# Performance work log

Measured on AMD Instinct MI355X. Metric: run time of the kernel, lower is better.

Reference implementation:

```python
import jax, jax.numpy as jnp
import numpy as np

N_NODES = 50000
N_EDGES = 1600000
D = 64  # per-node feature dim for h1 and h2


def setup_inputs() -> dict:
    key = jax.random.key(0)
    ks = jax.random.split(key, 8)
    h1 = jax.random.normal(ks[0], (N_NODES, D), dtype=jnp.float32)
    h2 = jax.random.normal(ks[1], (N_NODES, D), dtype=jnp.float32)
    src = jax.random.randint(ks[2], (N_EDGES,), 0, N_NODES)
    dst = jax.random.randint(ks[3], (N_EDGES,), 0, N_NODES)
    # MLP params: layer_sizes = [256, 128, 128, 1]
    def glorot(k, fan_in, fan_out):
        lim = (6.0 / (fan_in + fan_out)) ** 0.5
        return jax.random.uniform(k, (fan_in, fan_out), jnp.float32, -lim, lim)
    W0 = glorot(ks[4], 4 * D, 128)
    W1 = glorot(ks[5], 128, 128)
    W2 = glorot(ks[6], 128, 1)
    b0 = jnp.zeros((128,), jnp.float32)
    b1 = jnp.zeros((128,), jnp.float32)
    b2 = jnp.zeros((1,), jnp.float32)
    return {"h1": h1, "h2": h2, "src": src, "dst": dst,
            "W0": W0, "b0": b0, "W1": W1, "b1": b1, "W2": W2, "b2": b2}


def reference(h1, h2, src, dst, W0, b0, W1, b1, W2, b2):
    # Edge-wise gather of src/dst node features, concat -> MLP (eval mode: dropout=identity).
    h = jnp.concatenate([h1[src], h1[dst], h2[src], h2[dst]], axis=1)  # [E, 4D]
    h = h @ W0 + b0
    h = jax.nn.relu(h) @ W1 + b1
    h = jax.nn.relu(h) @ W2 + b2
    return h  # [E, out_features]
```

## Files before the change

kernel.cpp:

```cpp
#include <hip/hip_runtime.h>
#include <hip/hip_bf16.h>
#include <stdint.h>


typedef __attribute__((ext_vector_type(8))) __bf16 bf16x8;
typedef __attribute__((ext_vector_type(4))) __bf16 bf16x4;
typedef __attribute__((ext_vector_type(4))) float  floatx4;

__device__ inline floatx4 mfma16x16x32(bf16x8 a, bf16x8 b, floatx4 c) {
  return __builtin_amdgcn_mfma_f32_16x16x32_bf16(a, b, c, 0, 0, 0);
}

__device__ inline void bar_lds() {
  asm volatile("s_waitcnt lgkmcnt(0)" ::: "memory");
  __builtin_amdgcn_s_barrier();
}

__global__ void cvt_w_kernel(const float* __restrict__ W0, const float* __restrict__ W1,
                             __bf16* __restrict__ W1T, __bf16* __restrict__ W0uT,
                             __bf16* __restrict__ W0wT) {
  const int t = blockIdx.x * 256 + threadIdx.x;
  if (t < 16384) {
    const int n = t >> 7, k = t & 127;
    W1T[t] = (__bf16)W1[k * 128 + n];
  } else if (t < 32768) {
    const int t2 = t - 16384;
    const int n = t2 >> 7, k2 = t2 & 127;
    const int row = (k2 < 64) ? k2 : 64 + k2;
    W0uT[t2] = (__bf16)W0[row * 128 + n];
  } else {
    const int t3 = t - 32768;
    const int n = t3 >> 7, k2 = t3 & 127;
    const int row = (k2 < 64) ? 64 + k2 : 128 + k2;
    W0wT[t3] = (__bf16)W0[row * 128 + n];
  }
}

__global__ __launch_bounds__(256, 2)
void node_uw_kernel(const float* __restrict__ h1, const float* __restrict__ h2,
                    const __bf16* __restrict__ W0uT, const __bf16* __restrict__ W0wT,
                    const float* __restrict__ b0,
                    __bf16* __restrict__ uTab, __bf16* __restrict__ wTab, int nNodes) {
  __shared__ char sN[64 * 256];
  const int tid = threadIdx.x;
  const int base = blockIdx.x * 64;

  {
    const int r = tid >> 2, q = tid & 3;
    const int node = base + r;
    const int swz = (r & 7) << 4;
#pragma unroll
    for (int ii = 0; ii < 4; ++ii) {
      const int c = q * 4 + ii;
      bf16x8 v;
      if (node < nNodes) {
        const float* sp = (c < 8) ? (h1 + (size_t)node * 64 + c * 8)
                                  : (h2 + (size_t)node * 64 + (c - 8) * 8);
        const float4 x = reinterpret_cast<const float4*>(sp)[0];
        const float4 y = reinterpret_cast<const float4*>(sp)[1];
        v[0] = (__bf16)x.x; v[1] = (__bf16)x.y; v[2] = (__bf16)x.z; v[3] = (__bf16)x.w;
        v[4] = (__bf16)y.x; v[5] = (__bf16)y.y; v[6] = (__bf16)y.z; v[7] = (__bf16)y.w;
      } else {
#pragma unroll
        for (int k = 0; k < 8; ++k) v[k] = (__bf16)0.f;
      }
      *reinterpret_cast<bf16x8*>(sN + r * 256 + ((c * 16) ^ swz)) = v;
    }
  }
  __syncthreads();

  const int lane = tid & 63;
  const int l15 = lane & 15;
  const int hi = lane >> 4;
  const int hi16 = hi * 16;
  const int wvU = __builtin_amdgcn_readfirstlane(tid >> 6);

  float b0c[2][4];
#pragma unroll
  for (int nt = 0; nt < 2; ++nt)
#pragma unroll
    for (int r = 0; r < 4; ++r) b0c[nt][r] = b0[wvU * 32 + nt * 16 + hi * 4 + r];

#pragma unroll
  for (int pass = 0; pass < 2; ++pass) {
    const __bf16* Wt = pass ? W0wT : W0uT;
    __bf16* Tab = pass ? wTab : uTab;
    const bf16x8* wp = reinterpret_cast<const bf16x8*>(Wt);
    bf16x8 wf[4][2];
#pragma unroll
    for (int kk = 0; kk < 4; ++kk) {
      wf[kk][0] = wp[(wvU * 32 + l15) * 16 + kk * 4 + hi];
      wf[kk][1] = wp[(wvU * 32 + 16 + l15) * 16 + kk * 4 + hi];
    }
    floatx4 acc[4][2];
#pragma unroll
    for (int mt = 0; mt < 4; ++mt) { acc[mt][0] = (floatx4)0.f; acc[mt][1] = (floatx4)0.f; }
#pragma unroll
    for (int kk = 0; kk < 4; ++kk) {
#pragma unroll
      for (int mt = 0; mt < 4; ++mt) {
        const int row = mt * 16 + l15;
        const bf16x8 a = *reinterpret_cast<const bf16x8*>(
            sN + row * 256 + ((kk * 64 + hi16) ^ ((row & 7) << 4)));
        acc[mt][0] = mfma16x16x32(wf[kk][0], a, acc[mt][0]);
        acc[mt][1] = mfma16x16x32(wf[kk][1], a, acc[mt][1]);
      }
    }
#pragma unroll
    for (int mt = 0; mt < 4; ++mt) {
      const int node = base + mt * 16 + l15;
      if (node < nNodes) {
#pragma unroll
        for (int nt = 0; nt < 2; ++nt) {
          bf16x4 pk;
#pragma unroll
          for (int r = 0; r < 4; ++r) {
            const float v = acc[mt][nt][r] + (pass ? 0.f : b0c[nt][r]);
            pk[r] = (__bf16)v;
          }
          *reinterpret_cast<bf16x4*>(Tab + (size_t)node * 128 + wvU * 32 + nt * 16 +
                                     hi * 4) = pk;
        }
      }
    }
  }
}

__global__ __launch_bounds__(512, 2)
void edge_uw_kernel(const __bf16* __restrict__ uTab, const __bf16* __restrict__ wTab,
                    const int* __restrict__ srcI, const int* __restrict__ dstI,
                    const __bf16* __restrict__ W1T, const float* __restrict__ b1,
                    const float* __restrict__ W2, const float* __restrict__ b2,
                    float* __restrict__ out, int E, int nTiles) {
  __shared__ char sUW[2 * 64 * 512];
  __shared__ char sH[64 * 256];

  const int tid = threadIdx.x;
  const int lane = tid & 63;
  const int l15 = lane & 15;
  const int hi = lane >> 4;
  const int hi16 = hi * 16;
  const int wvU = __builtin_amdgcn_readfirstlane(tid >> 6);
  const int wm = wvU >> 2;
  const int wn = wvU & 3;
  const int wvByte = wvU * 4096;

  const int lhalf = lane >> 5;
  const int p31 = lane & 31;
  const int half = (p31 >> 4) & 1;
  const int* gIdxTab = half ? dstI : srcI;
  const __bf16* gTab = half ? wTab : uTab;

  bf16x8 w1f[4][2];
  const bf16x8* w1p = reinterpret_cast<const bf16x8*>(W1T);
#pragma unroll
  for (int kk = 0; kk < 4; ++kk) {
    w1f[kk][0] = w1p[(wn * 32 + l15) * 16 + kk * 4 + hi];
    w1f[kk][1] = w1p[(wn * 32 + 16 + l15) * 16 + kk * 4 + hi];
  }
  float b1c[2][4], w2c[2][4];
#pragma unroll
  for (int nt = 0; nt < 2; ++nt)
#pragma unroll
    for (int r = 0; r < 4; ++r) {
      const int n = wn * 32 + nt * 16 + hi * 4 + r;
      b1c[nt][r] = b1[n];
      w2c[nt][r] = W2[n];
    }
  const float b2v = b2[0];

  const int tstride = gridDim.x;

  auto loadIdx = [&](int (&d)[4], int tt2) {
    const bool valid = tt2 < nTiles;
#pragma unroll
    for (int i = 0; i < 4; ++i) {
      const int eLoc = wvU * 8 + i * 2 + lhalf;
      const int ge = tt2 * 64 + eLoc;
      d[i] = (valid && ge < E) ? gIdxTab[ge] : 0;
    }
  };

  auto issueGather = [&](int nb, const int (&idx4)[4]) {
#pragma unroll
    for (int i = 0; i < 4; ++i) {
      const int eLoc = wvU * 8 + i * 2 + lhalf;
      const int wc = (p31 & 8) | ((p31 & 7) ^ (eLoc & 7));
      const __bf16* g = gTab + (size_t)idx4[i] * 128 + wc * 8;
      char* l = sUW + nb * 32768 + wvByte + i * 1024;
      __builtin_amdgcn_global_load_lds(
          (const __attribute__((address_space(1))) void*)g,
          (__attribute__((address_space(3))) void*)l, 16, 0, 0);
    }
  };

  const int tile0 = blockIdx.x;
  int idxA[4], idxB[4];
  loadIdx(idxA, tile0);
  issueGather(0, idxA);
  loadIdx(idxB, tile0 + tstride);
  int cur = 0;

  for (int tt = tile0; tt < nTiles; tt += tstride) {
    __syncthreads();

    if (tt + tstride < nTiles) issueGather(cur ^ 1, idxB);
    loadIdx(idxA, tt + 2 * tstride);

    const char* sUWc = sUW + cur * 32768;

    {
      const int aR = tid >> 3;
      const int q = tid & 7;
      const int aswz = (aR & 7) << 4;
      const char* rowU = sUWc + aR * 512;
      char* rowH = sH + aR * 256;
#pragma unroll
      for (int ii = 0; ii < 2; ++ii) {
        const int c = q * 2 + ii;
        const int off = (c * 16) ^ aswz;
        const bf16x8 uu = *reinterpret_cast<const bf16x8*>(rowU + off);
        const bf16x8 ww = *reinterpret_cast<const bf16x8*>(rowU + 256 + off);
        bf16x8 hh;
#pragma unroll
        for (int k = 0; k < 8; ++k)
          hh[k] = (__bf16)fmaxf((float)uu[k] + (float)ww[k], 0.0f);
        *reinterpret_cast<bf16x8*>(rowH + off) = hh;
      }
    }
    bar_lds();

    floatx4 acc2T[2][2];
#pragma unroll
    for (int mt = 0; mt < 2; ++mt) { acc2T[mt][0] = (floatx4)0.f; acc2T[mt][1] = (floatx4)0.f; }
#pragma unroll
    for (int kk = 0; kk < 4; ++kk) {
#pragma unroll
      for (int mt = 0; mt < 2; ++mt) {
        const int row = wm * 32 + mt * 16 + l15;
        const bf16x8 a = *reinterpret_cast<const bf16x8*>(
            sH + row * 256 + ((kk * 64 + hi16) ^ ((row & 7) << 4)));
        acc2T[mt][0] = mfma16x16x32(w1f[kk][0], a, acc2T[mt][0]);
        acc2T[mt][1] = mfma16x16x32(w1f[kk][1], a, acc2T[mt][1]);
      }
    }

    float* sRedF = (float*)sUWc;
#pragma unroll
    for (int mt = 0; mt < 2; ++mt) {
      float pp = 0.f;
#pragma unroll
      for (int nt = 0; nt < 2; ++nt)
#pragma unroll
        for (int r = 0; r < 4; ++r)
          pp += fmaxf(acc2T[mt][nt][r] + b1c[nt][r], 0.0f) * w2c[nt][r];
      pp += __shfl_xor(pp, 16);
      pp += __shfl_xor(pp, 32);
      if (lane < 16) sRedF[(wm * 32 + mt * 16 + l15) * 4 + wn] = pp;
    }
    bar_lds();

    if (tid < 64) {
      const int ge = tt * 64 + tid;
      if (ge < E) {
        const float4 v = reinterpret_cast<const float4*>(sRedF)[tid];
        out[ge] = v.x + v.y + v.z + v.w + b2v;
      }
    }

#pragma unroll
    for (int i = 0; i < 4; ++i) idxB[i] = idxA[i];
    cur ^= 1;
  }
}

__global__ void edge_mlp_fallback(const float* __restrict__ h1, const float* __restrict__ h2,
                                  const int* __restrict__ src, const int* __restrict__ dst,
                                  const float* __restrict__ W0, const float* __restrict__ b0,
                                  const float* __restrict__ W1, const float* __restrict__ b1,
                                  const float* __restrict__ W2, const float* __restrict__ b2,
                                  float* __restrict__ out, int E) {
  __shared__ float sa[256];
  __shared__ float sh[128];
  __shared__ float sr[128];
  const int e = blockIdx.x;
  if (e >= E) return;
  const int t = threadIdx.x;
  const int is = src[e], id = dst[e];
  if (t < 64) { sa[t] = h1[is * 64 + t]; sa[128 + t] = h2[is * 64 + t]; }
  else { const int u = t - 64; sa[64 + u] = h1[id * 64 + u]; sa[192 + u] = h2[id * 64 + u]; }
  __syncthreads();
  float a0 = b0[t];
  for (int k = 0; k < 256; ++k) a0 += sa[k] * W0[k * 128 + t];
  sh[t] = fmaxf(a0, 0.f);
  __syncthreads();
  float a1 = b1[t];
  for (int k = 0; k < 128; ++k) a1 += sh[k] * W1[k * 128 + t];
  sr[t] = fmaxf(a1, 0.f) * W2[t];
  __syncthreads();
  if (t == 0) {
    float s = b2[0];
    for (int k = 0; k < 128; ++k) s += sr[k];
    out[e] = s;
  }
}

extern "C" void kernel_launch(void* const* d_in, const int* in_sizes, int n_in,
                              void* d_out, int out_size, void* d_ws, size_t ws_size,
                              hipStream_t stream) {
  const float* h1 = (const float*)d_in[0];
  const float* h2 = (const float*)d_in[1];
  const int* src = (const int*)d_in[2];
  const int* dst = (const int*)d_in[3];
  const float* W0 = (const float*)d_in[4];
  const float* b0 = (const float*)d_in[5];
  const float* W1 = (const float*)d_in[6];
  const float* b1 = (const float*)d_in[7];
  const float* W2 = (const float*)d_in[8];
  const float* b2 = (const float*)d_in[9];
  float* out = (float*)d_out;

  const int D = 64;
  const int nNodes = in_sizes[0] / D;
  const int E = in_sizes[2];

  char* ws = (char*)d_ws;
  __bf16* W1T = (__bf16*)(ws);
  __bf16* W0uT = (__bf16*)(ws + 32768);
  __bf16* W0wT = (__bf16*)(ws + 65536);
  const size_t tabBytes = (size_t)nNodes * 128 * sizeof(__bf16);
  __bf16* uTab = (__bf16*)(ws + 98304);
  __bf16* wTab = (__bf16*)(ws + 98304 + tabBytes);
  const bool useFast = ws_size >= 98304 + 2 * tabBytes;

  if (!useFast) {
    edge_mlp_fallback<<<dim3(E), dim3(128), 0, stream>>>(
        h1, h2, src, dst, W0, b0, W1, b1, W2, b2, out, E);
    return;
  }

  cvt_w_kernel<<<dim3(192), dim3(256), 0, stream>>>(W0, W1, W1T, W0uT, W0wT);
  node_uw_kernel<<<dim3((nNodes + 63) / 64), dim3(256), 0, stream>>>(
      h1, h2, W0uT, W0wT, b0, uTab, wTab, nNodes);

  const int nTiles = (E + 63) / 64;
  const int grid = nTiles < 512 ? nTiles : 512;
  edge_uw_kernel<<<dim3(grid), dim3(512), 0, stream>>>(
      uTab, wTab, src, dst, W1T, b1, W2, b2, out, E, nTiles);
}
```

Baseline: 151.7 us.

## Halve edge tile size, drop sH buffer, defer output write for higher occupancy

Edge tiles shrink from 64 to 32 edges, and the separate sH LDS buffer is dropped by writing the relu(u+w) result in place over the w half of the gather buffer. This cuts LDS per block so more blocks fit per CU. The second barrier per tile is removed by double-buffering the reduction array and writing the previous tile's outputs after the next iteration's sync, and launch bounds and grid size are raised to match. Smaller tiles mean less MFMA work per wave per tile and more per-tile overhead, and higher launch bounds may squeeze registers.

After: 345.7 us. 2.28x slower.

```diff
diff --git a/kernel.cpp b/kernel.cpp
--- a/kernel.cpp
+++ b/kernel.cpp
@@ -36,7 +36,7 @@
   }
 }
 
-__global__ __launch_bounds__(256, 2)
+__global__ __launch_bounds__(256, 4)
 void node_uw_kernel(const float* __restrict__ h1, const float* __restrict__ h2,
                     const __bf16* __restrict__ W0uT, const __bf16* __restrict__ W0wT,
                     const float* __restrict__ b0,
@@ -126,14 +126,14 @@
   }
 }
 
-__global__ __launch_bounds__(512, 2)
+__global__ __launch_bounds__(512, 6)
 void edge_uw_kernel(const __bf16* __restrict__ uTab, const __bf16* __restrict__ wTab,
                     const int* __restrict__ srcI, const int* __restrict__ dstI,
                     const __bf16* __restrict__ W1T, const float* __restrict__ b1,
                     const float* __restrict__ W2, const float* __restrict__ b2,
                     float* __restrict__ out, int E, int nTiles) {
-  __shared__ char sUW[2 * 64 * 512];
-  __shared__ char sH[64 * 256];
+  __shared__ char sUW[2 * 32 * 512];
+  __shared__ float sRed[2][32][4];
 
   const int tid = threadIdx.x;
   const int lane = tid & 63;
@@ -143,7 +143,6 @@
   const int wvU = __builtin_amdgcn_readfirstlane(tid >> 6);
   const int wm = wvU >> 2;
   const int wn = wvU & 3;
-  const int wvByte = wvU * 4096;
 
   const int lhalf = lane >> 5;
   const int p31 = lane & 31;
@@ -171,23 +170,23 @@
 
   const int tstride = gridDim.x;
 
-  auto loadIdx = [&](int (&d)[4], int tt2) {
+  auto loadIdx = [&](int (&d)[2], int tt2) {
     const bool valid = tt2 < nTiles;
 #pragma unroll
-    for (int i = 0; i < 4; ++i) {
-      const int eLoc = wvU * 8 + i * 2 + lhalf;
-      const int ge = tt2 * 64 + eLoc;
+    for (int i = 0; i < 2; ++i) {
+      const int eLoc = wvU * 4 + i * 2 + lhalf;
+      const int ge = tt2 * 32 + eLoc;
       d[i] = (valid && ge < E) ? gIdxTab[ge] : 0;
     }
   };
 
-  auto issueGather = [&](int nb, const int (&idx4)[4]) {
-#pragma unroll
-    for (int i = 0; i < 4; ++i) {
-      const int eLoc = wvU * 8 + i * 2 + lhalf;
+  auto issueGather = [&](int nb, const int (&idx2)[2]) {
+#pragma unroll
+    for (int i = 0; i < 2; ++i) {
+      const int eLoc = wvU * 4 + i * 2 + lhalf;
       const int wc = (p31 & 8) | ((p31 & 7) ^ (eLoc & 7));
-      const __bf16* g = gTab + (size_t)idx4[i] * 128 + wc * 8;
-      char* l = sUW + nb * 32768 + wvByte + i * 1024;
+      const __bf16* g = gTab + (size_t)idx2[i] * 128 + wc * 8;
+      char* l = sUW + nb * 16384 + wvU * 2048 + i * 1024;
       __builtin_amdgcn_global_load_lds(
           (const __attribute__((address_space(1))) void*)g,
           (__attribute__((address_space(3))) void*)l, 16, 0, 0);
@@ -195,82 +194,83 @@
   };
 
   const int tile0 = blockIdx.x;
-  int idxA[4], idxB[4];
+  int idxA[2], idxB[2];
   loadIdx(idxA, tile0);
   issueGather(0, idxA);
   loadIdx(idxB, tile0 + tstride);
   int cur = 0;
+  int prevBase = -1;
 
   for (int tt = tile0; tt < nTiles; tt += tstride) {
     __syncthreads();
 
+    if (prevBase >= 0 && tid < 32) {
+      const int ge = prevBase + tid;
+      if (ge < E) {
+        const float4 v = *reinterpret_cast<const float4*>(&sRed[cur ^ 1][tid][0]);
+        out[ge] = v.x + v.y + v.z + v.w + b2v;
+      }
+    }
+
     if (tt + tstride < nTiles) issueGather(cur ^ 1, idxB);
     loadIdx(idxA, tt + 2 * tstride);
 
-    const char* sUWc = sUW + cur * 32768;
+    char* sUWc = sUW + cur * 16384;
 
     {
-      const int aR = tid >> 3;
-      const int q = tid & 7;
-      const int aswz = (aR & 7) << 4;
-      const char* rowU = sUWc + aR * 512;
-      char* rowH = sH + aR * 256;
-#pragma unroll
-      for (int ii = 0; ii < 2; ++ii) {
-        const int c = q * 2 + ii;
-        const int off = (c * 16) ^ aswz;
-        const bf16x8 uu = *reinterpret_cast<const bf16x8*>(rowU + off);
-        const bf16x8 ww = *reinterpret_cast<const bf16x8*>(rowU + 256 + off);
-        bf16x8 hh;
-#pragma unroll
-        for (int k = 0; k < 8; ++k)
-          hh[k] = (__bf16)fmaxf((float)uu[k] + (float)ww[k], 0.0f);
-        *reinterpret_cast<bf16x8*>(rowH + off) = hh;
-      }
+      const int aR = tid >> 4;
+      const int c = tid & 15;
+      char* rowp = sUWc + aR * 512;
+      const int off = (c * 16) ^ ((aR & 7) << 4);
+      const bf16x8 uu = *reinterpret_cast<const bf16x8*>(rowp + off);
+      const bf16x8 ww = *reinterpret_cast<const bf16x8*>(rowp + 256 + off);
+      bf16x8 hh;
+#pragma unroll
+      for (int k = 0; k < 8; ++k)
+        hh[k] = (__bf16)fmaxf((float)uu[k] + (float)ww[k], 0.0f);
+      *reinterpret_cast<bf16x8*>(rowp + 256 + off) = hh;
     }
     bar_lds();
 
-    floatx4 acc2T[2][2];
-#pragma unroll
-    for (int mt = 0; mt < 2; ++mt) { acc2T[mt][0] = (floatx4)0.f; acc2T[mt][1] = (floatx4)0.f; }
-#pragma unroll
-    for (int kk = 0; kk < 4; ++kk) {
-#pragma unroll
-      for (int mt = 0; mt < 2; ++mt) {
-        const int row = wm * 32 + mt * 16 + l15;
-        const bf16x8 a = *reinterpret_cast<const bf16x8*>(
-            sH + row * 256 + ((kk * 64 + hi16) ^ ((row & 7) << 4)));
-        acc2T[mt][0] = mfma16x16x32(w1f[kk][0], a, acc2T[mt][0]);
-        acc2T[mt][1] = mfma16x16x32(w1f[kk][1], a, acc2T[mt][1]);
-      }
-    }
-
-    float* sRedF = (float*)sUWc;
-#pragma unroll
-    for (int mt = 0; mt < 2; ++mt) {
+    floatx4 acc0 = (floatx4)0.f, acc1 = (floatx4)0.f;
+    {
+      const int row = wm * 16 + l15;
+      const char* rowh = sUWc + row * 512 + 256;
+      const int rswz = (row & 7) << 4;
+#pragma unroll
+      for (int kk = 0; kk < 4; ++kk) {
+        const bf16x8 a =
+            *reinterpret_cast<const bf16x8*>(rowh + ((kk * 64 + hi16) ^ rswz));
+        acc0 = mfma16x16x32(w1f[kk][0], a, acc0);
+        acc1 = mfma16x16x32(w1f[kk][1], a, acc1);
+      }
+    }
+
+    {
       float pp = 0.f;
 #pragma unroll
-      for (int nt = 0; nt < 2; ++nt)
-#pragma unroll
-        for (int r = 0; r < 4; ++r)
-          pp += fmaxf(acc2T[mt][nt][r] + b1c[nt][r], 0.0f) * w2c[nt][r];
+      for (int r = 0; r < 4; ++r) {
+        pp += fmaxf(acc0[r] + b1c[0][r], 0.0f) * w2c[0][r];
+        pp += fmaxf(acc1[r] + b1c[1][r], 0.0f) * w2c[1][r];
+      }
       pp += __shfl_xor(pp, 16);
       pp += __shfl_xor(pp, 32);
-      if (lane < 16) sRedF[(wm * 32 + mt * 16 + l15) * 4 + wn] = pp;
-    }
-    bar_lds();
-
-    if (tid < 64) {
-      const int ge = tt * 64 + tid;
-      if (ge < E) {
-        const float4 v = reinterpret_cast<const float4*>(sRedF)[tid];
-        out[ge] = v.x + v.y + v.z + v.w + b2v;
-      }
-    }
-
-#pragma unroll
-    for (int i = 0; i < 4; ++i) idxB[i] = idxA[i];
+      if (lane < 16) sRed[cur][wm * 16 + l15][wn] = pp;
+    }
+
+    prevBase = tt * 32;
+    idxB[0] = idxA[0];
+    idxB[1] = idxA[1];
     cur ^= 1;
+  }
+
+  __syncthreads();
+  if (prevBase >= 0 && tid < 32) {
+    const int ge = prevBase + tid;
+    if (ge < E) {
+      const float4 v = *reinterpret_cast<const float4*>(&sRed[cur ^ 1][tid][0]);
+      out[ge] = v.x + v.y + v.z + v.w + b2v;
+    }
   }
 }
 
@@ -343,8 +343,8 @@
   node_uw_kernel<<<dim3((nNodes + 63) / 64), dim3(256), 0, stream>>>(
       h1, h2, W0uT, W0wT, b0, uTab, wTab, nNodes);
 
-  const int nTiles = (E + 63) / 64;
-  const int grid = nTiles < 512 ? nTiles : 512;
+  const int nTiles = (E + 31) / 32;
+  const int grid = nTiles < 1024 ? nTiles : 1024;
   edge_uw_kernel<<<dim3(grid), dim3(512), 0, stream>>>(
       uTab, wTab, src, dst, W1T, b1, W2, b2, out, E, nTiles);
 }
```

## Bucket edges by src/dst node range to localize gathers per block group

Applied to the files above, without the earlier changes.

Adds a histogram, scan and scatter pass that groups edges into 8x8 buckets by src and dst node range. Each group of blocks then processes only the buckets for one src range, so the gathered rows of the per-node tables come from a smaller working set that may stay in cache. This costs four extra kernel launches, extra passes over the indices and a scattered write of the output through a permutation. The sorted path runs only when the workspace is large enough, and blocks within a group work on spans of uneven length, which can cause load imbalance.

Result: slower. 207.8 us (+37.0%).

```diff
diff --git a/kernel.cpp b/kernel.cpp
--- a/kernel.cpp
+++ b/kernel.cpp
@@ -126,12 +126,87 @@
   }
 }
 
+__global__ void zero_cnt_kernel(int* __restrict__ cnt) {
+  if (threadIdx.x < 64) cnt[threadIdx.x] = 0;
+}
+
+__global__ void hist_kernel(const int* __restrict__ src, const int* __restrict__ dst,
+                            int* __restrict__ cnt, int E, int q) {
+  __shared__ int lc[64];
+  if (threadIdx.x < 64) lc[threadIdx.x] = 0;
+  __syncthreads();
+  const int base = blockIdx.x * 2048;
+#pragma unroll
+  for (int j = 0; j < 8; ++j) {
+    const int e = base + threadIdx.x + j * 256;
+    if (e < E) {
+      const int k = (src[e] / q) * 8 + dst[e] / q;
+      atomicAdd(&lc[k], 1);
+    }
+  }
+  __syncthreads();
+  if (threadIdx.x < 64 && lc[threadIdx.x]) atomicAdd(&cnt[threadIdx.x], lc[threadIdx.x]);
+}
+
+__global__ void scan_kernel(const int* __restrict__ cnt, int* __restrict__ offE,
+                            int* __restrict__ cur) {
+  if (threadIdx.x == 0) {
+    int run = 0;
+    for (int k = 0; k < 64; ++k) {
+      offE[k] = run;
+      cur[k] = run;
+      run += cnt[k];
+    }
+    offE[64] = run;
+  }
+}
+
+__global__ void scatter_kernel(const int* __restrict__ src, const int* __restrict__ dst,
+                               int* __restrict__ cur, int* __restrict__ srcP,
+                               int* __restrict__ dstP, int* __restrict__ eP,
+                               int E, int q) {
+  __shared__ int lc[64];
+  __shared__ int gb[64];
+  if (threadIdx.x < 64) lc[threadIdx.x] = 0;
+  __syncthreads();
+  const int base = blockIdx.x * 2048;
+  int myk[8], myr[8], mys[8], myd[8];
+#pragma unroll
+  for (int j = 0; j < 8; ++j) {
+    const int e = base + threadIdx.x + j * 256;
+    myk[j] = -1;
+    if (e < E) {
+      const int s = src[e], d = dst[e];
+      const int k = (s / q) * 8 + d / q;
+      myr[j] = atomicAdd(&lc[k], 1);
+      myk[j] = k; mys[j] = s; myd[j] = d;
+    }
+  }
+  __syncthreads();
+  if (threadIdx.x < 64) {
+    const int c = lc[threadIdx.x];
+    gb[threadIdx.x] = c ? atomicAdd(&cur[threadIdx.x], c) : 0;
+  }
+  __syncthreads();
+#pragma unroll
+  for (int j = 0; j < 8; ++j) {
+    if (myk[j] >= 0) {
+      const int pos = gb[myk[j]] + myr[j];
+      srcP[pos] = mys[j];
+      dstP[pos] = myd[j];
+      eP[pos] = base + threadIdx.x + j * 256;
+    }
+  }
+}
+
+template <bool SORTED>
 __global__ __launch_bounds__(512, 2)
 void edge_uw_kernel(const __bf16* __restrict__ uTab, const __bf16* __restrict__ wTab,
-                    const int* __restrict__ srcI, const int* __restrict__ dstI,
+                    const int* __restrict__ srcA, const int* __restrict__ dstA,
+                    const int* __restrict__ eP, const int* __restrict__ offE,
                     const __bf16* __restrict__ W1T, const float* __restrict__ b1,
                     const float* __restrict__ W2, const float* __restrict__ b2,
-                    float* __restrict__ out, int E, int nTiles) {
+                    float* __restrict__ out, int E) {
   __shared__ char sUW[2 * 64 * 512];
   __shared__ char sH[64 * 256];
 
@@ -143,12 +218,22 @@
   const int wvU = __builtin_amdgcn_readfirstlane(tid >> 6);
   const int wm = wvU >> 2;
   const int wn = wvU & 3;
-  const int wvByte = wvU * 4096;
+
+  int lo, hi_e, bOff, bStride;
+  if (SORTED) {
+    const int x = blockIdx.x & 7;
+    bOff = blockIdx.x >> 3;
+    bStride = gridDim.x >> 3;
+    lo = offE[x * 8];
+    hi_e = offE[x * 8 + 8];
+  } else {
+    lo = 0; hi_e = E; bOff = blockIdx.x; bStride = gridDim.x;
+  }
 
   const int lhalf = lane >> 5;
   const int p31 = lane & 31;
   const int half = (p31 >> 4) & 1;
-  const int* gIdxTab = half ? dstI : srcI;
+  const int* gIdxTab = half ? dstA : srcA;
   const __bf16* gTab = half ? wTab : uTab;
 
   bf16x8 w1f[4][2];
@@ -169,15 +254,12 @@
     }
   const float b2v = b2[0];
 
-  const int tstride = gridDim.x;
-
-  auto loadIdx = [&](int (&d)[4], int tt2) {
-    const bool valid = tt2 < nTiles;
+  auto loadIdx = [&](int (&d)[4], int ebase) {
 #pragma unroll
     for (int i = 0; i < 4; ++i) {
       const int eLoc = wvU * 8 + i * 2 + lhalf;
-      const int ge = tt2 * 64 + eLoc;
-      d[i] = (valid && ge < E) ? gIdxTab[ge] : 0;
+      const int ge = ebase + eLoc;
+      d[i] = (ge < hi_e) ? gIdxTab[ge] : 0;
     }
   };
 
@@ -187,27 +269,28 @@
       const int eLoc = wvU * 8 + i * 2 + lhalf;
       const int wc = (p31 & 8) | ((p31 & 7) ^ (eLoc & 7));
       const __bf16* g = gTab + (size_t)idx4[i] * 128 + wc * 8;
-      char* l = sUW + nb * 32768 + wvByte + i * 1024;
+      char* l = sUW + nb * 32768 + wvU * 4096 + i * 1024;
       __builtin_amdgcn_global_load_lds(
           (const __attribute__((address_space(1))) void*)g,
           (__attribute__((address_space(3))) void*)l, 16, 0, 0);
     }
   };
 
-  const int tile0 = blockIdx.x;
+  const int tb0 = lo + bOff * 64;
+  const int tstep = bStride * 64;
   int idxA[4], idxB[4];
-  loadIdx(idxA, tile0);
+  loadIdx(idxA, tb0);
   issueGather(0, idxA);
-  loadIdx(idxB, tile0 + tstride);
+  loadIdx(idxB, tb0 + tstep);
   int cur = 0;
 
-  for (int tt = tile0; tt < nTiles; tt += tstride) {
+  for (int tb = tb0; tb < hi_e; tb += tstep) {
     __syncthreads();
 
-    if (tt + tstride < nTiles) issueGather(cur ^ 1, idxB);
-    loadIdx(idxA, tt + 2 * tstride);
-
-    const char* sUWc = sUW + cur * 32768;
+    if (tb + tstep < hi_e) issueGather(cur ^ 1, idxB);
+    loadIdx(idxA, tb + 2 * tstep);
+
+    char* sUWc = sUW + cur * 32768;
 
     {
       const int aR = tid >> 3;
@@ -261,10 +344,11 @@
     bar_lds();
 
     if (tid < 64) {
-      const int ge = tt * 64 + tid;
-      if (ge < E) {
+      const int ge = tb + tid;
+      if (ge < hi_e) {
         const float4 v = reinterpret_cast<const float4*>(sRedF)[tid];
-        out[ge] = v.x + v.y + v.z + v.w + b2v;
+        const float r = v.x + v.y + v.z + v.w + b2v;
+        if (SORTED) out[eP[ge]] = r; else out[ge] = r;
       }
     }
 
@@ -331,7 +415,16 @@
   const size_t tabBytes = (size_t)nNodes * 128 * sizeof(__bf16);
   __bf16* uTab = (__bf16*)(ws + 98304);
   __bf16* wTab = (__bf16*)(ws + 98304 + tabBytes);
+  size_t off = 98304 + 2 * tabBytes;
+  int* srcP = (int*)(ws + off); off += (size_t)E * 4;
+  int* dstP = (int*)(ws + off); off += (size_t)E * 4;
+  int* ePrm = (int*)(ws + off); off += (size_t)E * 4;
+  int* cnt  = (int*)(ws + off); off += 256;
+  int* offE = (int*)(ws + off); off += 512;
+  int* curC = (int*)(ws + off); off += 256;
+
   const bool useFast = ws_size >= 98304 + 2 * tabBytes;
+  const bool useSort = ws_size >= off;
 
   if (!useFast) {
     edge_mlp_fallback<<<dim3(E), dim3(128), 0, stream>>>(
@@ -343,8 +436,20 @@
   node_uw_kernel<<<dim3((nNodes + 63) / 64), dim3(256), 0, stream>>>(
       h1, h2, W0uT, W0wT, b0, uTab, wTab, nNodes);
 
-  const int nTiles = (E + 63) / 64;
-  const int grid = nTiles < 512 ? nTiles : 512;
-  edge_uw_kernel<<<dim3(grid), dim3(512), 0, stream>>>(
-      uTab, wTab, src, dst, W1T, b1, W2, b2, out, E, nTiles);
-}
+  if (useSort) {
+    const int q = (nNodes + 7) / 8;
+    const int nChunk = (E + 2047) / 2048;
+    zero_cnt_kernel<<<dim3(1), dim3(64), 0, stream>>>(cnt);
+    hist_kernel<<<dim3(nChunk), dim3(256), 0, stream>>>(src, dst, cnt, E, q);
+    scan_kernel<<<dim3(1), dim3(64), 0, stream>>>(cnt, offE, curC);
+    scatter_kernel<<<dim3(nChunk), dim3(256), 0, stream>>>(src, dst, curC, srcP, dstP,
+                                                           ePrm, E, q);
+    edge_uw_kernel<true><<<dim3(512), dim3(512), 0, stream>>>(
+        uTab, wTab, srcP, dstP, ePrm, offE, W1T, b1, W2, b2, out, E);
+  } else {
+    const int nTiles = (E + 63) / 64;
+    const int grid = nTiles < 512 ? nTiles : 512;
+    edge_uw_kernel<false><<<dim3(grid), dim3(512), 0, stream>>>(
+        uTab, wTab, src, dst, nullptr, nullptr, W1T, b1, W2, b2, out, E);
+  }
+}
```
